# Kernel optimization log

Measured on AMD Instinct MI355X. Metric: run time of the kernel, lower is better.

The kernel has to match this reference:

```python
import jax, jax.numpy as jnp
import numpy as np

DIM = 512
HEADS = 8
DIM_HEAD = 64
HIDDEN = HEADS * DIM_HEAD  # 512
B, C, H, W = 32, DIM, 32, 32


def setup_inputs() -> dict:
    key = jax.random.key(0)
    ks = jax.random.split(key, 7)
    s_in = 1.0 / np.sqrt(DIM)
    s_h = 1.0 / np.sqrt(HIDDEN)
    x = jax.random.normal(ks[0], (B, C, H, W), dtype=jnp.float32)
    Wq = jax.random.uniform(ks[1], (DIM, HIDDEN), jnp.float32, -s_in, s_in)
    Wk = jax.random.uniform(ks[2], (DIM, HIDDEN), jnp.float32, -s_in, s_in)
    Wv = jax.random.uniform(ks[3], (DIM, HIDDEN), jnp.float32, -s_in, s_in)
    Wp = jax.random.uniform(ks[4], (HIDDEN, DIM), jnp.float32, -s_h, s_h)
    bp = jax.random.uniform(ks[5], (DIM,), jnp.float32, -s_h, s_h)
    return {"x": x, "Wq": Wq, "Wk": Wk, "Wv": Wv, "Wp": Wp, "bp": bp}


def reference(x, Wq, Wk, Wv, Wp, bp):
    b, c, h, w = x.shape
    n = h * w
    xt = x.reshape(b, c, n).transpose(0, 2, 1)  # [B, N, C]
    q = (xt @ Wq).reshape(b, n, HEADS, DIM_HEAD)
    k = (xt @ Wk).reshape(b, n, HEADS, DIM_HEAD)
    v = (xt @ Wv).reshape(b, n, HEADS, DIM_HEAD)
    k_softmax = jax.nn.softmax(k, axis=1)  # softmax over tokens N
    context = jnp.einsum('bnhd,bnhv->bhdv', k_softmax, v)  # [B, H, D, D]
    out = jnp.einsum('bnhd,bhdv->bnhv', q, context).reshape(b, n, HIDDEN)
    out = out @ Wp + bp  # [B, N, C]
    return out.transpose(0, 2, 1).reshape(b, c, h, w)
```

## Files before the change

kernel.cpp:

```cpp
#include <hip/hip_runtime.h>
#include <hip/hip_bf16.h>


__device__ __forceinline__ float bf2f(unsigned short u) {
    union { unsigned int i; float f; } x;
    x.i = ((unsigned int)u) << 16;
    return x.f;
}
__device__ __forceinline__ unsigned short f2bf(float f) {
    unsigned int u = __float_as_uint(f);
    unsigned int lsb = (u >> 16) & 1u;
    u += 0x7fffu + lsb;
    return (unsigned short)(u >> 16);
}

__device__ __forceinline__ void glds16(const unsigned short* g, unsigned short* l) {
    __builtin_amdgcn_global_load_lds(
        (const __attribute__((address_space(1))) unsigned int*)g,
        (__attribute__((address_space(3))) unsigned int*)l,
        16, 0, 0);
}

typedef __bf16 bf16x8 __attribute__((ext_vector_type(8)));
typedef float  f32x4  __attribute__((ext_vector_type(4)));

__global__ void detect_dtype(const unsigned short* __restrict__ x, int* __restrict__ flag)
{
    int t = threadIdx.x;
    unsigned short u = x[2 * t];
    int e = (u >> 7) & 0xFF;
    int sane = (e >= 113 && e <= 142) ? 1 : 0;
    #pragma unroll
    for (int off = 32; off > 0; off >>= 1) sane += __shfl_xor(sane, off, 64);
    if (t == 0) *flag = (sane >= 32) ? 1 : 0;
}

__global__ __launch_bounds__(256) void transpose_x(
    const void* __restrict__ in, unsigned short* __restrict__ out,
    const int* __restrict__ flag)
{
    const int fl = *flag;
    const int b  = blockIdx.z;
    const int c0 = blockIdx.x * 64;
    const int r0 = blockIdx.y * 64;
    __shared__ unsigned short Ts[64][68];
    const int t   = threadIdx.x;
    const int tr  = t >> 4;
    const int tc4 = (t & 15) * 4;
    #pragma unroll
    for (int rr = 0; rr < 4; ++rr) {
        int rl = rr * 16 + tr;
        long off = (long)b * 524288 + (long)(r0 + rl) * 1024 + c0 + tc4;
        unsigned short v[4];
        if (fl) {
            ushort4 u = *(const ushort4*)((const unsigned short*)in + off);
            v[0] = u.x; v[1] = u.y; v[2] = u.z; v[3] = u.w;
        } else {
            float4 u = *(const float4*)((const float*)in + off);
            v[0] = f2bf(u.x); v[1] = f2bf(u.y); v[2] = f2bf(u.z); v[3] = f2bf(u.w);
        }
        #pragma unroll
        for (int q = 0; q < 4; ++q) Ts[tc4 + q][rl] = v[q];
    }
    __syncthreads();
    #pragma unroll
    for (int rr = 0; rr < 4; ++rr) {
        int cl = rr * 16 + tr;
        ushort4 o = *(const ushort4*)&Ts[cl][tc4];
        *(ushort4*)(out + (long)b * 524288 + (long)(c0 + cl) * 512 + r0 + tc4) = o;
    }
}

__global__ __launch_bounds__(256) void transpose_w3(
    const void* __restrict__ w0, const void* __restrict__ w1,
    const void* __restrict__ w2, unsigned short* __restrict__ out,
    unsigned short* __restrict__ wqb,
    const int* __restrict__ flag)
{
    const int fl = *flag;
    const int z  = blockIdx.z;
    const void* in = (z == 0) ? w0 : (z == 1) ? w1 : w2;
    unsigned short* op = out + (long)z * 262144;
    const int c0 = blockIdx.x * 64;
    const int r0 = blockIdx.y * 64;
    __shared__ unsigned short Ts[64][68];
    const int t   = threadIdx.x;
    const int tr  = t >> 4;
    const int tc4 = (t & 15) * 4;
    #pragma unroll
    for (int rr = 0; rr < 4; ++rr) {
        int rl = rr * 16 + tr;
        long off = (long)(r0 + rl) * 512 + c0 + tc4;
        unsigned short v[4];
        if (fl) {
            ushort4 u = *(const ushort4*)((const unsigned short*)in + off);
            v[0] = u.x; v[1] = u.y; v[2] = u.z; v[3] = u.w;
        } else {
            float4 u = *(const float4*)((const float*)in + off);
            v[0] = f2bf(u.x); v[1] = f2bf(u.y); v[2] = f2bf(u.z); v[3] = f2bf(u.w);
        }
        if (z == 0) {
            ushort4 s; s.x = v[0]; s.y = v[1]; s.z = v[2]; s.w = v[3];
            *(ushort4*)(wqb + off) = s;
        }
        #pragma unroll
        for (int q = 0; q < 4; ++q) Ts[tc4 + q][rl] = v[q];
    }
    __syncthreads();
    #pragma unroll
    for (int rr = 0; rr < 4; ++rr) {
        int cl = rr * 16 + tr;
        ushort4 o = *(const ushort4*)&Ts[cl][tc4];
        *(ushort4*)(op + (long)(c0 + cl) * 512 + r0 + tc4) = o;
    }
}

__global__ __launch_bounds__(1024, 4) void gemm_bt_256(
    const unsigned short* __restrict__ A, long a_bstride,
    const unsigned short* __restrict__ Bm, long b_bstride,
    void* __restrict__ C, long c_bstride,
    const void* __restrict__ bias,
    int M, int N, int K, int mode,
    const int* __restrict__ flag)
{
    const int b  = blockIdx.z;
    const int n0 = blockIdx.x * 256;
    const int m0 = blockIdx.y * 256;
    const unsigned short* Ab = A  + (long)b * a_bstride;
    const unsigned short* Bb = Bm + (long)b * b_bstride;

    __shared__ unsigned short S[65536];

    const int t  = threadIdx.x;
    const int w  = t >> 6;
    const int l  = t & 63;
    const int fm = l & 15;
    const int kg = l >> 4;
    const int wr = w >> 2;
    const int wc = w & 3;

    const int rowb = w * 8 + (l >> 3);
    const int swz  = ((l & 7) ^ (l >> 3)) * 8;
    const unsigned short* gA = Ab + (long)(m0 + rowb) * K + swz;
    const unsigned short* gB = Bb + (long)(n0 + rowb) * K + swz;

    const int sA = fm & 7;

    f32x4 acc[4][4] = {};

    const int NT = K >> 6;

    auto STAGE = [&](int kt, int buf) {
        const long ko = (long)kt * 64;
        unsigned short* Ld = &S[buf * 32768];
        #pragma unroll
        for (int r = 0; r < 2; ++r)
            glds16(gA + (long)r * 128 * K + ko, Ld + (r * 128 + w * 8) * 64);
        #pragma unroll
        for (int r = 0; r < 2; ++r)
            glds16(gB + (long)r * 128 * K + ko, Ld + 16384 + (r * 128 + w * 8) * 64);
    };

    STAGE(0, 0);

    for (int tt = 0; tt < NT; ++tt) {
        if (tt + 1 < NT) {
            STAGE(tt + 1, (tt + 1) & 1);
            __builtin_amdgcn_sched_barrier(0);
            asm volatile("s_waitcnt vmcnt(4)" ::: "memory");
        } else {
            __builtin_amdgcn_sched_barrier(0);
            asm volatile("s_waitcnt vmcnt(0)" ::: "memory");
        }
        __builtin_amdgcn_sched_barrier(0);
        __builtin_amdgcn_s_barrier();
        __builtin_amdgcn_sched_barrier(0);

        {
            const unsigned short* Abuf = &S[(tt & 1) * 32768];
            const unsigned short* Bbuf = Abuf + 16384;
            bf16x8 bf[4][2];
            #pragma unroll
            for (int j = 0; j < 4; ++j)
                #pragma unroll
                for (int kk = 0; kk < 2; ++kk) {
                    const int row = wc * 64 + j * 16 + fm;
                    bf[j][kk] = *(const bf16x8*)&Bbuf[row * 64 + ((kk * 4 + kg) ^ sA) * 8];
                }
            #pragma unroll
            for (int i = 0; i < 4; ++i) {
                bf16x8 af[2];
                #pragma unroll
                for (int kk = 0; kk < 2; ++kk) {
                    const int row = wr * 64 + i * 16 + fm;
                    af[kk] = *(const bf16x8*)&Abuf[row * 64 + ((kk * 4 + kg) ^ sA) * 8];
                }
                __builtin_amdgcn_s_setprio(1);
                #pragma unroll
                for (int j = 0; j < 4; ++j)
                    #pragma unroll
                    for (int kk = 0; kk < 2; ++kk)
                        acc[i][j] = __builtin_amdgcn_mfma_f32_16x16x32_bf16(
                            bf[j][kk], af[kk], acc[i][j], 0, 0, 0);
                __builtin_amdgcn_s_setprio(0);
            }
        }

        __builtin_amdgcn_sched_barrier(0);
        __builtin_amdgcn_s_barrier();
        __builtin_amdgcn_sched_barrier(0);
    }

    const int fl = *flag;
    const long cb = (long)b * c_bstride;
    #pragma unroll
    for (int i = 0; i < 4; ++i) {
        const int m = m0 + wr * 64 + i * 16 + fm;
        float bv = 0.f;
        if (mode == 2 && bias)
            bv = fl ? bf2f(((const unsigned short*)bias)[m])
                    : ((const float*)bias)[m];
        #pragma unroll
        for (int j = 0; j < 4; ++j) {
            const int nb = n0 + wc * 64 + j * 16 + kg * 4;
            const long off = cb + (long)m * N + nb;
            if (mode == 0) {
                ushort4 o;
                o.x = f2bf(acc[i][j][0]); o.y = f2bf(acc[i][j][1]);
                o.z = f2bf(acc[i][j][2]); o.w = f2bf(acc[i][j][3]);
                *(ushort4*)&((unsigned short*)C)[off] = o;
            } else if (fl) {
                ushort4 o;
                o.x = f2bf(acc[i][j][0] + bv); o.y = f2bf(acc[i][j][1] + bv);
                o.z = f2bf(acc[i][j][2] + bv); o.w = f2bf(acc[i][j][3] + bv);
                *(ushort4*)&((unsigned short*)C)[off] = o;
            } else {
                float4 o;
                o.x = acc[i][j][0] + bv; o.y = acc[i][j][1] + bv;
                o.z = acc[i][j][2] + bv; o.w = acc[i][j][3] + bv;
                *(float4*)&((float*)C)[off] = o;
            }
        }
    }
}

__global__ __launch_bounds__(256) void gemm_bt_mfma(
    const unsigned short* __restrict__ A, long a_bstride,
    const unsigned short* __restrict__ Bm, long b_bstride,
    void* __restrict__ C, long c_bstride,
    const void* __restrict__ bias,
    int M, int N, int K, int mode,
    const int* __restrict__ flag)
{
    const int b  = blockIdx.z;
    const int n0 = blockIdx.x * 128;
    const int m0 = blockIdx.y * 128;
    const unsigned short* Ab = A  + (long)b * a_bstride;
    const unsigned short* Bb = Bm + (long)b * b_bstride;

    __shared__ unsigned short As[2 * 128 * 32];
    __shared__ unsigned short Bs[2 * 128 * 32];

    const int t    = threadIdx.x;
    const int w    = t >> 6;
    const int lane = t & 63;
    const int wm   = (w & 1) * 64;
    const int wn   = (w >> 1) * 64;
    const int fm   = lane & 15;
    const int kg   = lane >> 4;

    const int crow = lane >> 2;
    const int ccol = (lane & 3) * 8;

    f32x4 acc[4][4] = {};

    #pragma unroll
    for (int j = 0; j < 2; ++j) {
        const int chunk = w * 2 + j;
        const int row   = chunk * 16 + crow;
        glds16(Ab + (long)(m0 + row) * K + ccol, &As[chunk * 512]);
        glds16(Bb + (long)(n0 + row) * K + ccol, &Bs[chunk * 512]);
    }

    int cur = 0;
    for (int k0 = 0; k0 < K; k0 += 32) {
        __syncthreads();

        if (k0 + 32 < K) {
            const int kn  = k0 + 32;
            const int nxt = (cur ^ 1) * 4096;
            #pragma unroll
            for (int j = 0; j < 2; ++j) {
                const int chunk = w * 2 + j;
                const int row   = chunk * 16 + crow;
                glds16(Ab + (long)(m0 + row) * K + kn + ccol, &As[nxt + chunk * 512]);
                glds16(Bb + (long)(n0 + row) * K + kn + ccol, &Bs[nxt + chunk * 512]);
            }
        }

        const int bufo = cur * 4096;
        bf16x8 af[4], bf[4];
        #pragma unroll
        for (int i = 0; i < 4; ++i)
            af[i] = *(const bf16x8*)&As[bufo + (wm + i * 16 + fm) * 32 + kg * 8];
        #pragma unroll
        for (int j = 0; j < 4; ++j)
            bf[j] = *(const bf16x8*)&Bs[bufo + (wn + j * 16 + fm) * 32 + kg * 8];
        #pragma unroll
        for (int i = 0; i < 4; ++i)
            #pragma unroll
            for (int j = 0; j < 4; ++j)
                acc[i][j] = __builtin_amdgcn_mfma_f32_16x16x32_bf16(
                    bf[j], af[i], acc[i][j], 0, 0, 0);
        cur ^= 1;
    }

    const int fl = *flag;
    const long cb = (long)b * c_bstride;
    #pragma unroll
    for (int i = 0; i < 4; ++i) {
        const int m = m0 + wm + i * 16 + fm;
        float bv = 0.f;
        if (mode == 2 && bias)
            bv = fl ? bf2f(((const unsigned short*)bias)[m])
                    : ((const float*)bias)[m];
        #pragma unroll
        for (int j = 0; j < 4; ++j) {
            const int nb = n0 + wn + j * 16 + kg * 4;
            const long off = cb + (long)m * N + nb;
            if (mode == 0) {
                ushort4 o;
                o.x = f2bf(acc[i][j][0]); o.y = f2bf(acc[i][j][1]);
                o.z = f2bf(acc[i][j][2]); o.w = f2bf(acc[i][j][3]);
                *(ushort4*)&((unsigned short*)C)[off] = o;
            } else if (fl) {
                ushort4 o;
                o.x = f2bf(acc[i][j][0] + bv); o.y = f2bf(acc[i][j][1] + bv);
                o.z = f2bf(acc[i][j][2] + bv); o.w = f2bf(acc[i][j][3] + bv);
                *(ushort4*)&((unsigned short*)C)[off] = o;
            } else {
                float4 o;
                o.x = acc[i][j][0] + bv; o.y = acc[i][j][1] + bv;
                o.z = acc[i][j][2] + bv; o.w = acc[i][j][3] + bv;
                *(float4*)&((float*)C)[off] = o;
            }
        }
    }
}

__global__ __launch_bounds__(256) void ctx_softmax_mfma(
    const unsigned short* __restrict__ KV, float* __restrict__ ctx)
{
    const int bh = blockIdx.x;
    const unsigned short* Kb = KV + ((long)(bh >> 3) << 20) + (long)(bh & 7) * 65536;
    const unsigned short* Vb = Kb + 524288;

    const int t    = threadIdx.x;
    const int w    = t >> 6;
    const int lane = t & 63;
    const int fm   = lane & 15;
    const int kg   = lane >> 4;

    __shared__ float sm_m[64];
    __shared__ float sm_inv[64];

    {
        const int r = t >> 2;
        const int q = t & 3;
        const uint4* row = (const uint4*)(Kb + r * 1024 + q * 256);
        float mx = -3.402823466e+38f;
        #pragma unroll 8
        for (int i = 0; i < 32; ++i) {
            uint4 u = row[i];
            #pragma unroll
            for (int z = 0; z < 4; ++z) {
                unsigned int uu = ((const unsigned int*)&u)[z];
                float lo = bf2f((unsigned short)(uu & 0xffffu));
                float hi = bf2f((unsigned short)(uu >> 16));
                mx = fmaxf(mx, fmaxf(lo, hi));
            }
        }
        mx = fmaxf(mx, __shfl_xor(mx, 1, 64));
        mx = fmaxf(mx, __shfl_xor(mx, 2, 64));
        float s = 0.f;
        #pragma unroll 8
        for (int i = 0; i < 32; ++i) {
            uint4 u = row[i];
            #pragma unroll
            for (int z = 0; z < 4; ++z) {
                unsigned int uu = ((const unsigned int*)&u)[z];
                s += __expf(bf2f((unsigned short)(uu & 0xffffu)) - mx);
                s += __expf(bf2f((unsigned short)(uu >> 16)) - mx);
            }
        }
        s += __shfl_xor(s, 1, 64);
        s += __shfl_xor(s, 2, 64);
        if (q == 0) { sm_m[r] = mx; sm_inv[r] = 1.0f / s; }
    }
    __syncthreads();

    float rm[4], ri[4];
    #pragma unroll
    for (int i = 0; i < 4; ++i) {
        rm[i] = sm_m[i * 16 + fm];
        ri[i] = sm_inv[i * 16 + fm];
    }

    f32x4 acc[4][4] = {};

    #pragma unroll 2
    for (int c = 0; c < 8; ++c) {
        const int k0 = w * 256 + c * 32;
        bf16x8 af[4], bf[4];
        #pragma unroll
        for (int i = 0; i < 4; ++i) {
            uint4 u = *(const uint4*)(Kb + (long)(i * 16 + fm) * 1024 + k0 + kg * 8);
            unsigned short o[8];
            #pragma unroll
            for (int z = 0; z < 4; ++z) {
                unsigned int uu = ((const unsigned int*)&u)[z];
                float lo = __expf(bf2f((unsigned short)(uu & 0xffffu)) - rm[i]) * ri[i];
                float hi = __expf(bf2f((unsigned short)(uu >> 16))     - rm[i]) * ri[i];
                o[2 * z]     = f2bf(lo);
                o[2 * z + 1] = f2bf(hi);
            }
            af[i] = *(const bf16x8*)o;
        }
        #pragma unroll
        for (int j = 0; j < 4; ++j)
            bf[j] = *(const bf16x8*)(Vb + (long)(j * 16 + fm) * 1024 + k0 + kg * 8);
        #pragma unroll
        for (int i = 0; i < 4; ++i)
            #pragma unroll
            for (int j = 0; j < 4; ++j)
                acc[i][j] = __builtin_amdgcn_mfma_f32_16x16x32_bf16(
                    af[i], bf[j], acc[i][j], 0, 0, 0);
    }

    __shared__ float red[64][65];
    for (int ph = 0; ph < 4; ++ph) {
        if (w == ph) {
            #pragma unroll
            for (int i = 0; i < 4; ++i)
                #pragma unroll
                for (int j = 0; j < 4; ++j)
                    #pragma unroll
                    for (int r = 0; r < 4; ++r) {
                        const int m = i * 16 + kg * 4 + r;
                        const int n = j * 16 + fm;
                        if (ph == 0) red[m][n]  = acc[i][j][r];
                        else         red[m][n] += acc[i][j][r];
                    }
        }
        __syncthreads();
    }
    float* cp = ctx + (long)bh * 4096;
    for (int i = t; i < 4096; i += 256) cp[i] = red[i >> 6][i & 63];
}

__global__ __launch_bounds__(256) void weff_kernel(
    const float* __restrict__ ctx,
    const void* __restrict__ Wp,
    unsigned short* __restrict__ WeffT,
    const int* __restrict__ flag)
{
    const int fl = *flag;
    const int c0 = blockIdx.x * 64;
    const int h  = blockIdx.y;
    const int b  = blockIdx.z;

    __shared__ float Cs[64][65];
    __shared__ float Ws[64][68];

    const int t = threadIdx.x;
    const int tx = t & 15, ty = t >> 4;

    const float* cb = ctx + ((long)b * 8 + h) * 4096;
    for (int i = t; i < 4096; i += 256) Cs[i >> 6][i & 63] = cb[i];
    for (int i = t; i < 4096; i += 256) {
        int v = i >> 6, c = i & 63;
        long idx = (long)(h * 64 + v) * 512 + c0 + c;
        Ws[v][c] = fl ? bf2f(((const unsigned short*)Wp)[idx])
                      : ((const float*)Wp)[idx];
    }
    __syncthreads();

    float acc[4][4];
    #pragma unroll
    for (int i = 0; i < 4; ++i)
        #pragma unroll
        for (int j = 0; j < 4; ++j) acc[i][j] = 0.f;

    #pragma unroll
    for (int v = 0; v < 64; ++v) {
        float a[4], d[4];
        #pragma unroll
        for (int i = 0; i < 4; ++i) a[i] = Ws[v][ty * 4 + i];
        #pragma unroll
        for (int j = 0; j < 4; ++j) d[j] = Cs[tx * 4 + j][v];
        #pragma unroll
        for (int i = 0; i < 4; ++i)
            #pragma unroll
            for (int j = 0; j < 4; ++j) acc[i][j] += a[i] * d[j];
    }
    #pragma unroll
    for (int i = 0; i < 4; ++i) {
        ushort4 o;
        o.x = f2bf(acc[i][0]); o.y = f2bf(acc[i][1]);
        o.z = f2bf(acc[i][2]); o.w = f2bf(acc[i][3]);
        *(ushort4*)&WeffT[((long)b * 512 + c0 + ty * 4 + i) * 512 + h * 64 + tx * 4] = o;
    }
}

extern "C" void kernel_launch(void* const* d_in, const int* in_sizes, int n_in,
                              void* d_out, int out_size, void* d_ws, size_t ws_size,
                              hipStream_t stream) {
    const void* x  = d_in[0];
    const void* Wq = d_in[1];
    const void* Wk = d_in[2];
    const void* Wv = d_in[3];
    const void* Wp = d_in[4];
    const void* bp = d_in[5];

    char* ws = (char*)d_ws;
    unsigned short* Xt    = (unsigned short*)(ws);
    unsigned short* KV    = (unsigned short*)(ws + 33554432ll);
    unsigned short* Ft    = (unsigned short*)(ws + 33554432ll);
    float*          ctx   = (float*)(ws + 100663296ll);
    unsigned short* WeffT = (unsigned short*)(ws + 104857600ll);
    unsigned short* WT    = (unsigned short*)(ws + 121634816ll);
    unsigned short* Wqb   = (unsigned short*)(ws + 123207680ll);
    int*            flag  = (int*)(ws + 123731968ll);

    detect_dtype<<<dim3(1), dim3(64), 0, stream>>>((const unsigned short*)x, flag);

    transpose_x<<<dim3(16, 8, 32), 256, 0, stream>>>(x, Xt, flag);
    transpose_w3<<<dim3(8, 8, 3), 256, 0, stream>>>(Wq, Wk, Wv, WT, Wqb, flag);

    const long XB = 1024ll * 512;
    gemm_bt_256<<<dim3(4, 4, 32), 1024, 0, stream>>>(
        WT + 262144, 0, Xt, XB, KV, 1048576ll, nullptr, 1024, 1024, 512, 0, flag);

    ctx_softmax_mfma<<<dim3(256), 256, 0, stream>>>(KV, ctx);

    weff_kernel<<<dim3(8, 8, 32), 256, 0, stream>>>(ctx, Wp, WeffT, flag);

    gemm_bt_mfma<<<dim3(4, 4, 32), 256, 0, stream>>>(
        WeffT, 262144ll, Wqb, 0, Ft, 262144ll, nullptr, 512, 512, 512, 0, flag);

    gemm_bt_256<<<dim3(4, 2, 32), 1024, 0, stream>>>(
        Ft, 262144ll, Xt, XB, d_out, 524288ll, bp, 512, 1024, 512, 2, flag);
}
```

Before: 300.6 us.

## Single-pass softmax context, fold dtype detect into transpose, swizzle GEMM blocks

The context kernel no longer runs a separate max and sum pass over K. It exponentiates K without subtracting the max, accumulates the row sums alongside the MFMA loop, and applies the 1/sum normalization when writing the context. The standalone dtype-detection launch is folded into transpose_x, where each block recomputes the flag via a ballot and block 0 stores it. gemm_bt_256 remaps workgroup IDs so neighbouring tiles are spread across XCDs, aiming for better cache locality. Skipping the max subtraction risks exp overflow if K values are large, and computing exp before the bf16 cast changes rounding slightly.

```diff
diff --git a/kernel.cpp b/kernel.cpp
--- a/kernel.cpp
+++ b/kernel.cpp
@@ -24,27 +24,23 @@
 typedef __bf16 bf16x8 __attribute__((ext_vector_type(8)));
 typedef float  f32x4  __attribute__((ext_vector_type(4)));
 
-__global__ void detect_dtype(const unsigned short* __restrict__ x, int* __restrict__ flag)
-{
-    int t = threadIdx.x;
-    unsigned short u = x[2 * t];
-    int e = (u >> 7) & 0xFF;
-    int sane = (e >= 113 && e <= 142) ? 1 : 0;
-    #pragma unroll
-    for (int off = 32; off > 0; off >>= 1) sane += __shfl_xor(sane, off, 64);
-    if (t == 0) *flag = (sane >= 32) ? 1 : 0;
-}
-
 __global__ __launch_bounds__(256) void transpose_x(
     const void* __restrict__ in, unsigned short* __restrict__ out,
-    const int* __restrict__ flag)
+    int* __restrict__ flag)
 {
-    const int fl = *flag;
+    const int t = threadIdx.x;
+    const unsigned short* xs = (const unsigned short*)in;
+    unsigned short u0 = xs[2 * (t & 63)];
+    int e0 = (u0 >> 7) & 0xFF;
+    unsigned long long bm = __ballot(e0 >= 113 && e0 <= 142);
+    const int fl = (__popcll(bm) >= 32) ? 1 : 0;
+    if (blockIdx.x == 0 && blockIdx.y == 0 && blockIdx.z == 0 && t == 0)
+        *flag = fl;
+
     const int b  = blockIdx.z;
     const int c0 = blockIdx.x * 64;
     const int r0 = blockIdx.y * 64;
     __shared__ unsigned short Ts[64][68];
-    const int t   = threadIdx.x;
     const int tr  = t >> 4;
     const int tc4 = (t & 15) * 4;
     #pragma unroll
@@ -123,9 +119,17 @@
     int M, int N, int K, int mode,
     const int* __restrict__ flag)
 {
-    const int b  = blockIdx.z;
-    const int n0 = blockIdx.x * 256;
-    const int m0 = blockIdx.y * 256;
+    const int gx = gridDim.x, gy = gridDim.y;
+    const int nwg = gx * gy * (int)gridDim.z;
+    const int lid = blockIdx.x + gx * (blockIdx.y + gy * blockIdx.z);
+    const int swzid = (lid & 7) * (nwg >> 3) + (lid >> 3);
+    const int bx = swzid % gx;
+    const int by = (swzid / gx) % gy;
+    const int bz = swzid / (gx * gy);
+
+    const int b  = bz;
+    const int n0 = bx * 256;
+    const int m0 = by * 256;
     const unsigned short* Ab = A  + (long)b * a_bstride;
     const unsigned short* Bb = Bm + (long)b * b_bstride;
 
@@ -361,52 +365,8 @@
     const int fm   = lane & 15;
     const int kg   = lane >> 4;
 
-    __shared__ float sm_m[64];
-    __shared__ float sm_inv[64];
-
-    {
-        const int r = t >> 2;
-        const int q = t & 3;
-        const uint4* row = (const uint4*)(Kb + r * 1024 + q * 256);
-        float mx = -3.402823466e+38f;
-        #pragma unroll 8
-        for (int i = 0; i < 32; ++i) {
-            uint4 u = row[i];
-            #pragma unroll
-            for (int z = 0; z < 4; ++z) {
-                unsigned int uu = ((const unsigned int*)&u)[z];
-                float lo = bf2f((unsigned short)(uu & 0xffffu));
-                float hi = bf2f((unsigned short)(uu >> 16));
-                mx = fmaxf(mx, fmaxf(lo, hi));
-            }
-        }
-        mx = fmaxf(mx, __shfl_xor(mx, 1, 64));
-        mx = fmaxf(mx, __shfl_xor(mx, 2, 64));
-        float s = 0.f;
-        #pragma unroll 8
-        for (int i = 0; i < 32; ++i) {
-            uint4 u = row[i];
-            #pragma unroll
-            for (int z = 0; z < 4; ++z) {
-                unsigned int uu = ((const unsigned int*)&u)[z];
-                s += __expf(bf2f((unsigned short)(uu & 0xffffu)) - mx);
-                s += __expf(bf2f((unsigned short)(uu >> 16)) - mx);
-            }
-        }
-        s += __shfl_xor(s, 1, 64);
-        s += __shfl_xor(s, 2, 64);
-        if (q == 0) { sm_m[r] = mx; sm_inv[r] = 1.0f / s; }
-    }
-    __syncthreads();
-
-    float rm[4], ri[4];
-    #pragma unroll
-    for (int i = 0; i < 4; ++i) {
-        rm[i] = sm_m[i * 16 + fm];
-        ri[i] = sm_inv[i * 16 + fm];
-    }
-
     f32x4 acc[4][4] = {};
+    float sloc[4] = {0.f, 0.f, 0.f, 0.f};
 
     #pragma unroll 2
     for (int c = 0; c < 8; ++c) {
@@ -419,8 +379,9 @@
             #pragma unroll
             for (int z = 0; z < 4; ++z) {
                 unsigned int uu = ((const unsigned int*)&u)[z];
-                float lo = __expf(bf2f((unsigned short)(uu & 0xffffu)) - rm[i]) * ri[i];
-                float hi = __expf(bf2f((unsigned short)(uu >> 16))     - rm[i]) * ri[i];
+                float lo = __expf(bf2f((unsigned short)(uu & 0xffffu)));
+                float hi = __expf(bf2f((unsigned short)(uu >> 16)));
+                sloc[i] += lo + hi;
                 o[2 * z]     = f2bf(lo);
                 o[2 * z + 1] = f2bf(hi);
             }
@@ -437,8 +398,23 @@
                     af[i], bf[j], acc[i][j], 0, 0, 0);
     }
 
+    __shared__ float sred[4][64];
+    __shared__ float sinv[64];
+    #pragma unroll
+    for (int i = 0; i < 4; ++i) {
+        sloc[i] += __shfl_xor(sloc[i], 16, 64);
+        sloc[i] += __shfl_xor(sloc[i], 32, 64);
+    }
+    if (kg == 0) {
+        #pragma unroll
+        for (int i = 0; i < 4; ++i) sred[w][i * 16 + fm] = sloc[i];
+    }
+    __syncthreads();
+    if (t < 64) sinv[t] = 1.0f / (sred[0][t] + sred[1][t] + sred[2][t] + sred[3][t]);
+
     __shared__ float red[64][65];
     for (int ph = 0; ph < 4; ++ph) {
+        __syncthreads();
         if (w == ph) {
             #pragma unroll
             for (int i = 0; i < 4; ++i)
@@ -452,10 +428,11 @@
                         else         red[m][n] += acc[i][j][r];
                     }
         }
-        __syncthreads();
-    }
+    }
+    __syncthreads();
     float* cp = ctx + (long)bh * 4096;
-    for (int i = t; i < 4096; i += 256) cp[i] = red[i >> 6][i & 63];
+    for (int i = t; i < 4096; i += 256)
+        cp[i] = red[i >> 6][i & 63] * sinv[i >> 6];
 }
 
 __global__ __launch_bounds__(256) void weff_kernel(
@@ -532,8 +509,6 @@
     unsigned short* Wqb   = (unsigned short*)(ws + 123207680ll);
     int*            flag  = (int*)(ws + 123731968ll);
 
-    detect_dtype<<<dim3(1), dim3(64), 0, stream>>>((const unsigned short*)x, flag);
-
     transpose_x<<<dim3(16, 8, 32), 256, 0, stream>>>(x, Xt, flag);
     transpose_w3<<<dim3(8, 8, 3), 256, 0, stream>>>(Wq, Wk, Wv, WT, Wqb, flag);
 
```

New measurement: 284.1 us, median of 3. 5.5% less time.
